# Optimization experiments

Measured on AMD Instinct MI355X. Metric: run time of the kernel, lower is better.

The kernel has to match this reference:

```python
import jax, jax.numpy as jnp
import numpy as np
from jax import lax

DIM = 128
NUM_HEADS = 8
GROUP_SPLIT = (4, 4)
DIM_HEAD = DIM // NUM_HEADS  # 16
SCALOR = DIM_HEAD ** (-0.5)
KSIZE = 5
WS = 4
C_HI = GROUP_SPLIT[0] * DIM_HEAD  # 64
C_LO = GROUP_SPLIT[1] * DIM_HEAD  # 64


def conv1x1(x, w, b):
    # x: [b,c,h,w], w: [o,c], b: [o]
    return jnp.einsum('oc,bchw->bohw', w, x) + b[None, :, None, None]


def dwconv(x, w, b):
    # depthwise conv, w: [C,1,k,k]
    C = x.shape[1]
    pad = KSIZE // 2
    y = lax.conv_general_dilated(x, w, window_strides=(1, 1),
                                 padding=((pad, pad), (pad, pad)),
                                 dimension_numbers=('NCHW', 'OIHW', 'NCHW'),
                                 feature_group_count=C)
    return y + b[None, :, None, None]


def avgpool(x, ws):
    b, c, h, w = x.shape
    return x.reshape(b, c, h // ws, ws, w // ws, ws).mean(axis=(3, 5))


def setup_inputs() -> dict:
    key = jax.random.key(0)
    ks = jax.random.split(key, 16)
    s = 0.02
    inp = {
        'x': jax.random.normal(ks[0], (8, DIM, 96, 96), dtype=jnp.float32),
        'qkv_w': jax.random.normal(ks[1], (3 * C_HI, DIM), dtype=jnp.float32) * s,
        'qkv_b': jnp.zeros((3 * C_HI,), jnp.float32),
        'dw_w': jax.random.normal(ks[2], (3 * C_HI, 1, KSIZE, KSIZE), dtype=jnp.float32) * s,
        'dw_b': jnp.zeros((3 * C_HI,), jnp.float32),
        'am_w1': jax.random.normal(ks[3], (C_HI, C_HI), dtype=jnp.float32) * s,
        'am_b1': jnp.zeros((C_HI,), jnp.float32),
        'am_w2': jax.random.normal(ks[4], (C_HI, C_HI), dtype=jnp.float32) * s,
        'am_b2': jnp.zeros((C_HI,), jnp.float32),
        'gq_w': jax.random.normal(ks[5], (C_LO, DIM), dtype=jnp.float32) * s,
        'gq_b': jnp.zeros((C_LO,), jnp.float32),
        'gkv_w': jax.random.normal(ks[6], (2 * C_LO, DIM), dtype=jnp.float32) * s,
        'gkv_b': jnp.zeros((2 * C_LO,), jnp.float32),
        'proj_w': jax.random.normal(ks[7], (DIM, DIM), dtype=jnp.float32) * s,
        'proj_b': jnp.zeros((DIM,), jnp.float32),
    }
    return inp


def reference(x, qkv_w, qkv_b, dw_w, dw_b, am_w1, am_b1, am_w2, am_b2,
              gq_w, gq_b, gkv_w, gkv_b, proj_w, proj_b):
    b, c, h, w = x.shape
    # ---- high-frequency branch ----
    qkv = dwconv(conv1x1(x, qkv_w, qkv_b), dw_w, dw_b)  # [b, 3*C_HI, h, w]
    qkv = qkv.reshape(b, 3, C_HI, h, w)
    q, k, v = qkv[:, 0], qkv[:, 1], qkv[:, 2]
    a = conv1x1(q * k, am_w1, am_b1)
    a = a * jax.nn.sigmoid(a)  # swish
    a = conv1x1(a, am_w2, am_b2) * SCALOR
    hi = jnp.tanh(a) * v  # [b, C_HI, h, w]
    # ---- low-frequency (windowed global) branch ----
    nq = h * w
    nk = nq // (WS * WS)
    q = conv1x1(x, gq_w, gq_b).reshape(b, GROUP_SPLIT[1], DIM_HEAD, nq)
    q = q.transpose(0, 1, 3, 2)  # [b, H, nq, dh]
    kv = conv1x1(avgpool(x, WS), gkv_w, gkv_b)  # [b, 2*C_LO, h/ws, w/ws]
    kv = kv.reshape(b, 2, GROUP_SPLIT[1], DIM_HEAD, nk)
    kk = kv[:, 0].transpose(0, 1, 3, 2)  # [b, H, nk, dh]
    vv = kv[:, 1].transpose(0, 1, 3, 2)
    attn = jax.nn.softmax(SCALOR * jnp.einsum('bhqd,bhkd->bhqk', q, kk), axis=-1)
    lo = jnp.einsum('bhqk,bhkd->bhqd', attn, vv)  # [b, H, nq, dh]
    lo = lo.transpose(0, 1, 3, 2).reshape(b, C_LO, h, w)
    # ---- merge + projection ----
    out = jnp.concatenate([hi, lo], axis=1)
    return conv1x1(out, proj_w, proj_b)
```

## Files before the change

### kernel.cpp

```cpp
#include <hip/hip_runtime.h>
#include <hip/hip_bf16.h>
#include <hip/hip_fp16.h>
#include <cstdint>

static constexpr int NB  = 8;
static constexpr int HH  = 96;
static constexpr int WW  = 96;
static constexpr int NP  = 9216;
static constexpr int NPK = 576;

using bf8 = __attribute__((ext_vector_type(8))) short;
using f4  = __attribute__((ext_vector_type(4))) float;

__device__ __forceinline__ unsigned pack_bf2(float a, float b) {
    __hip_bfloat162 h = __float22bfloat162_rn(make_float2(a, b));
    unsigned u; __builtin_memcpy(&u, &h, 4);
    return u;
}
__device__ __forceinline__ unsigned short f2bfu(float f) {
    __hip_bfloat16 h = __float2bfloat16(f);
    unsigned short u; __builtin_memcpy(&u, &h, 2);
    return u;
}
__device__ __forceinline__ float bf2f(unsigned short u) {
    unsigned v = (unsigned)u << 16;
    float f; __builtin_memcpy(&f, &v, 4);
    return f;
}
__device__ __forceinline__ float bflo(unsigned p) {
    unsigned v = p << 16; float f; __builtin_memcpy(&f, &v, 4); return f;
}
__device__ __forceinline__ float bfhi(unsigned p) {
    unsigned v = p & 0xffff0000u; float f; __builtin_memcpy(&f, &v, 4); return f;
}

__global__ __launch_bounds__(256) void k_qkvgq(
    const float* __restrict__ x,
    const float* __restrict__ qkv_w, const float* __restrict__ qkv_b,
    const float* __restrict__ gq_w,  const float* __restrict__ gq_b,
    unsigned short* __restrict__ qkv_out,
    unsigned short* __restrict__ gq_out)
{
    __shared__ __align__(16) unsigned xl[64 * 64];
    const int tid  = threadIdx.x;
    const int lane = tid & 63, wid = tid >> 6;
    const int quad = blockIdx.x, b = blockIdx.z;
    const int arow = lane & 15, agrp = lane >> 4;

    const float* xb = x + (long long)b * 128 * NP + quad * 64;

#pragma unroll
    for (int it = 0; it < 4; ++it) {
        const int task = tid + 256 * it;
        const int cp = task >> 4, pq = task & 15;
        float4 a = *(const float4*)&xb[(long long)(2 * cp) * NP + pq * 4];
        float4 c = *(const float4*)&xb[(long long)(2 * cp + 1) * NP + pq * 4];
        const int cps = cp ^ ((pq & 7) << 2);
        xl[(pq * 4 + 0) * 64 + cps] = pack_bf2(a.x, c.x);
        xl[(pq * 4 + 1) * 64 + cps] = pack_bf2(a.y, c.y);
        xl[(pq * 4 + 2) * 64 + cps] = pack_bf2(a.z, c.z);
        xl[(pq * 4 + 3) * 64 + cps] = pack_bf2(a.w, c.w);
    }
    __syncthreads();

    uint4 breg[4][4];
#pragma unroll
    for (int kt = 0; kt < 4; ++kt)
#pragma unroll
        for (int i = 0; i < 4; ++i) {
            const int px = arow * 4 + i;
            const int cp = (kt * 16 + agrp * 4) ^ ((arow & 7) << 2);
            breg[kt][i] = *(const uint4*)&xl[px * 64 + cp];
        }

    for (int gi = 0; gi < 4; ++gi) {
        const int grp = wid + gi * 4;
        const bool isgq = grp >= 12;
        const float* wsrc = isgq ? gq_w : qkv_w;
        const float* bsrc = isgq ? gq_b : qkv_b;
        const float wsc = isgq ? 0.25f : 1.0f;
        const int och = (isgq ? grp - 12 : grp) * 16;

        bf8 afr[4];
#pragma unroll
        for (int kt = 0; kt < 4; ++kt) {
            const float* wp = wsrc + (long long)(och + arow) * 128 + kt * 32 + agrp * 8;
            int4 t;
            t.x = (int)pack_bf2(wp[0] * wsc, wp[1] * wsc);
            t.y = (int)pack_bf2(wp[2] * wsc, wp[3] * wsc);
            t.z = (int)pack_bf2(wp[4] * wsc, wp[5] * wsc);
            t.w = (int)pack_bf2(wp[6] * wsc, wp[7] * wsc);
            afr[kt] = __builtin_bit_cast(bf8, t);
        }

        f4 acc[4];
#pragma unroll
        for (int i = 0; i < 4; ++i) acc[i] = (f4){0.f, 0.f, 0.f, 0.f};
#pragma unroll
        for (int kt = 0; kt < 4; ++kt)
#pragma unroll
            for (int i = 0; i < 4; ++i)
                acc[i] = __builtin_amdgcn_mfma_f32_16x16x32_bf16(
                    afr[kt], __builtin_bit_cast(bf8, breg[kt][i]), acc[i], 0, 0, 0);

        unsigned short* ob = isgq ? gq_out : qkv_out;
        const int ostride = isgq ? 64 : 192;
#pragma unroll
        for (int r = 0; r < 4; ++r) {
            const int o = och + agrp * 4 + r;
            const float bs = bsrc[o] * wsc;
            const float v0 = acc[0][r] + bs, v1 = acc[1][r] + bs;
            const float v2 = acc[2][r] + bs, v3 = acc[3][r] + bs;
            *(uint2*)&ob[((long long)b * ostride + o) * NP + quad * 64 + arow * 4] =
                make_uint2(pack_bf2(v0, v1), pack_bf2(v2, v3));
        }
    }
}

template<int C, int OT, int INBF, int OUTBF>
__global__ __launch_bounds__(256) void k_mfma_conv(
    const void* __restrict__ in0v, const float* __restrict__ w,
    const float* __restrict__ bias, void* __restrict__ outv,
    int np, long long ibs, int storeO, float wscale)
{
    constexpr int KT = C / 32;
    const int tid  = threadIdx.x;
    const int lane = tid & 63, wid = tid >> 6;
    const int b    = blockIdx.z;
    const int obq  = blockIdx.y * (OT * 16);
    const int arow = lane & 15, agrp = lane >> 4;
    const int nquad = np >> 6;

    bf8 afr[OT][KT];
#pragma unroll
    for (int ot = 0; ot < OT; ++ot)
#pragma unroll
        for (int kt = 0; kt < KT; ++kt) {
            const float* wp = w + (long long)(obq + ot * 16 + arow) * C + kt * 32 + agrp * 8;
            int4 t;
            t.x = (int)pack_bf2(wp[0] * wscale, wp[1] * wscale);
            t.y = (int)pack_bf2(wp[2] * wscale, wp[3] * wscale);
            t.z = (int)pack_bf2(wp[4] * wscale, wp[5] * wscale);
            t.w = (int)pack_bf2(wp[6] * wscale, wp[7] * wscale);
            afr[ot][kt] = __builtin_bit_cast(bf8, t);
        }

    const float*          x0f = (const float*)in0v          + (long long)b * (INBF ? 0 : ibs);
    const unsigned short* x0h = (const unsigned short*)in0v + (long long)b * (INBF ? ibs : 0);

    const int quad = blockIdx.x * 4 + wid;
    if (quad >= nquad) return;
    const int p0 = quad * 64 + arow * 4;

    f4 acc[4][OT];
#pragma unroll
    for (int i = 0; i < 4; ++i)
#pragma unroll
        for (int ot = 0; ot < OT; ++ot) acc[i][ot] = (f4){0.f, 0.f, 0.f, 0.f};

#pragma unroll
    for (int kt = 0; kt < KT; ++kt) {
        const long long cbase = kt * 32 + agrp * 8;
        int uu[4][4];
#pragma unroll
        for (int jj = 0; jj < 4; ++jj) {
            if (INBF == 0) {
                float4 a0 = *(const float4*)&x0f[(cbase + 2 * jj) * np + p0];
                float4 a1 = *(const float4*)&x0f[(cbase + 2 * jj + 1) * np + p0];
                uu[0][jj] = (int)pack_bf2(a0.x, a1.x);
                uu[1][jj] = (int)pack_bf2(a0.y, a1.y);
                uu[2][jj] = (int)pack_bf2(a0.z, a1.z);
                uu[3][jj] = (int)pack_bf2(a0.w, a1.w);
            } else {
                ushort4 a0 = *(const ushort4*)&x0h[(cbase + 2 * jj) * np + p0];
                ushort4 a1 = *(const ushort4*)&x0h[(cbase + 2 * jj + 1) * np + p0];
                uu[0][jj] = (int)((unsigned)a0.x | ((unsigned)a1.x << 16));
                uu[1][jj] = (int)((unsigned)a0.y | ((unsigned)a1.y << 16));
                uu[2][jj] = (int)((unsigned)a0.z | ((unsigned)a1.z << 16));
                uu[3][jj] = (int)((unsigned)a0.w | ((unsigned)a1.w << 16));
            }
        }
#pragma unroll
        for (int i = 0; i < 4; ++i) {
            int4 ti = {uu[i][0], uu[i][1], uu[i][2], uu[i][3]};
            bf8 bfr = __builtin_bit_cast(bf8, ti);
#pragma unroll
            for (int ot = 0; ot < OT; ++ot)
                acc[i][ot] = __builtin_amdgcn_mfma_f32_16x16x32_bf16(afr[ot][kt], bfr, acc[i][ot], 0, 0, 0);
        }
    }

#pragma unroll
    for (int ot = 0; ot < OT; ++ot) {
#pragma unroll
        for (int r = 0; r < 4; ++r) {
            const int o = obq + ot * 16 + agrp * 4 + r;
            const float bs = bias[o] * wscale;
            float4 v;
            v.x = acc[0][ot][r] + bs;
            v.y = acc[1][ot][r] + bs;
            v.z = acc[2][ot][r] + bs;
            v.w = acc[3][ot][r] + bs;
            const long long idx = ((long long)b * storeO + o) * np + p0;
            if (OUTBF == 0) {
                *(float4*)&((float*)outv)[idx] = v;
            } else {
                *(uint2*)&((unsigned short*)outv)[idx] =
                    make_uint2(pack_bf2(v.x, v.y), pack_bf2(v.z, v.w));
            }
        }
    }
}

__global__ __launch_bounds__(256) void k_am_fused(
    const unsigned short* __restrict__ dw,
    const float* __restrict__ w1, const float* __restrict__ b1v,
    const float* __restrict__ w2, const float* __restrict__ b2v,
    unsigned short* __restrict__ hi)
{
    __shared__ __align__(16) uint2 abuf[4][1024];

    const int tid  = threadIdx.x;
    const int lane = tid & 63, wid = tid >> 6;
    const int b    = blockIdx.z;
    const int arow = lane & 15, agrp = lane >> 4;

    bf8 afr1[4][2], afr2[4][2];
#pragma unroll
    for (int ot = 0; ot < 4; ++ot)
#pragma unroll
        for (int kt = 0; kt < 2; ++kt) {
            const float* wp1 = w1 + (long long)(ot * 16 + arow) * 64 + kt * 32 + agrp * 8;
            const float* wp2 = w2 + (long long)(ot * 16 + arow) * 64 + kt * 32 + agrp * 8;
            int4 t1, t2;
            t1.x = (int)pack_bf2(wp1[0], wp1[1]);  t2.x = (int)pack_bf2(wp2[0], wp2[1]);
            t1.y = (int)pack_bf2(wp1[2], wp1[3]);  t2.y = (int)pack_bf2(wp2[2], wp2[3]);
            t1.z = (int)pack_bf2(wp1[4], wp1[5]);  t2.z = (int)pack_bf2(wp2[4], wp2[5]);
            t1.w = (int)pack_bf2(wp1[6], wp1[7]);  t2.w = (int)pack_bf2(wp2[6], wp2[7]);
            afr1[ot][kt] = __builtin_bit_cast(bf8, t1);
            afr2[ot][kt] = __builtin_bit_cast(bf8, t2);
        }

    const unsigned short* xq = dw + (long long)b * (192ll * NP);
    const unsigned short* xk = xq + 64ll * NP;
    const unsigned short* xv = xq + 128ll * NP;

    const int quad = blockIdx.x * 4 + wid;
    const int p0 = quad * 64 + arow * 4;

    f4 acc1[4][4];
#pragma unroll
    for (int i = 0; i < 4; ++i)
#pragma unroll
        for (int ot = 0; ot < 4; ++ot) acc1[i][ot] = (f4){0.f, 0.f, 0.f, 0.f};

#pragma unroll
    for (int kt = 0; kt < 2; ++kt) {
        const long long cbase = kt * 32 + agrp * 8;
        int uu[4][4];
#pragma unroll
        for (int jj = 0; jj < 4; ++jj) {
            ushort4 a0 = *(const ushort4*)&xq[(cbase + 2 * jj) * NP + p0];
            ushort4 a1 = *(const ushort4*)&xq[(cbase + 2 * jj + 1) * NP + p0];
            ushort4 y0 = *(const ushort4*)&xk[(cbase + 2 * jj) * NP + p0];
            ushort4 y1 = *(const ushort4*)&xk[(cbase + 2 * jj + 1) * NP + p0];
            uu[0][jj] = (int)pack_bf2(bf2f(a0.x) * bf2f(y0.x), bf2f(a1.x) * bf2f(y1.x));
            uu[1][jj] = (int)pack_bf2(bf2f(a0.y) * bf2f(y0.y), bf2f(a1.y) * bf2f(y1.y));
            uu[2][jj] = (int)pack_bf2(bf2f(a0.z) * bf2f(y0.z), bf2f(a1.z) * bf2f(y1.z));
            uu[3][jj] = (int)pack_bf2(bf2f(a0.w) * bf2f(y0.w), bf2f(a1.w) * bf2f(y1.w));
        }
#pragma unroll
        for (int i = 0; i < 4; ++i) {
            int4 ti = {uu[i][0], uu[i][1], uu[i][2], uu[i][3]};
            bf8 bfr = __builtin_bit_cast(bf8, ti);
#pragma unroll
            for (int ot = 0; ot < 4; ++ot)
                acc1[i][ot] = __builtin_amdgcn_mfma_f32_16x16x32_bf16(afr1[ot][kt], bfr, acc1[i][ot], 0, 0, 0);
        }
    }

#pragma unroll
    for (int i = 0; i < 4; ++i)
#pragma unroll
        for (int ot = 0; ot < 4; ++ot) {
            const int ch0 = ot * 16 + agrp * 4;
            float v0 = acc1[i][ot][0] + b1v[ch0 + 0];
            float v1 = acc1[i][ot][1] + b1v[ch0 + 1];
            float v2 = acc1[i][ot][2] + b1v[ch0 + 2];
            float v3 = acc1[i][ot][3] + b1v[ch0 + 3];
            v0 = v0 / (1.f + __expf(-v0));
            v1 = v1 / (1.f + __expf(-v1));
            v2 = v2 / (1.f + __expf(-v2));
            v3 = v3 / (1.f + __expf(-v3));
            const int c2 = ot * 4 + agrp;
            abuf[wid][(arow * 4 + i) * 16 + (c2 ^ arow)] =
                make_uint2(pack_bf2(v0, v1), pack_bf2(v2, v3));
        }

    f4 acc2[4][4];
#pragma unroll
    for (int i = 0; i < 4; ++i)
#pragma unroll
        for (int ot = 0; ot < 4; ++ot) acc2[i][ot] = (f4){0.f, 0.f, 0.f, 0.f};

#pragma unroll
    for (int kt = 0; kt < 2; ++kt) {
        const int bc2 = kt * 8 + agrp * 2;
#pragma unroll
        for (int i = 0; i < 4; ++i) {
            const uint2 rA = abuf[wid][(arow * 4 + i) * 16 + (bc2 ^ arow)];
            const uint2 rB = abuf[wid][(arow * 4 + i) * 16 + ((bc2 + 1) ^ arow)];
            int4 ti = make_int4((int)rA.x, (int)rA.y, (int)rB.x, (int)rB.y);
            bf8 bfr = __builtin_bit_cast(bf8, ti);
#pragma unroll
            for (int ot = 0; ot < 4; ++ot)
                acc2[i][ot] = __builtin_amdgcn_mfma_f32_16x16x32_bf16(afr2[ot][kt], bfr, acc2[i][ot], 0, 0, 0);
        }
    }

#pragma unroll
    for (int ot = 0; ot < 4; ++ot) {
#pragma unroll
        for (int r = 0; r < 4; ++r) {
            const int o = ot * 16 + agrp * 4 + r;
            const float bs = b2v[o];
            ushort4 vv4 = *(const ushort4*)&xv[(long long)o * NP + p0];
            float h0 = tanhf((acc2[0][ot][r] + bs) * 0.25f) * bf2f(vv4.x);
            float h1 = tanhf((acc2[1][ot][r] + bs) * 0.25f) * bf2f(vv4.y);
            float h2 = tanhf((acc2[2][ot][r] + bs) * 0.25f) * bf2f(vv4.z);
            float h3 = tanhf((acc2[3][ot][r] + bs) * 0.25f) * bf2f(vv4.w);
            *(uint2*)&hi[((long long)b * 128 + o) * NP + p0] =
                make_uint2(pack_bf2(h0, h1), pack_bf2(h2, h3));
        }
    }
}

__global__ __launch_bounds__(256) void k_dwconv5_lds(
    const unsigned short* __restrict__ in, const float* __restrict__ w,
    const float* __restrict__ bias, unsigned short* __restrict__ out, int ch_total)
{
    __shared__ __align__(16) float img[NP];
    const int tid = threadIdx.x;
    const int ch  = blockIdx.x;
    const int b   = blockIdx.y;
    const unsigned short* ip = in + ((long long)b * ch_total + ch) * NP;

#pragma unroll
    for (int j = 0; j < 9; ++j) {
        const uint2 rr = ((const uint2*)ip)[tid + 256 * j];
        float4 f;
        f.x = bflo(rr.x); f.y = bfhi(rr.x);
        f.z = bflo(rr.y); f.w = bfhi(rr.y);
        ((float4*)img)[tid + 256 * j] = f;
    }
    __syncthreads();

    const float* wp = w + ch * 25;
    float wr[25];
#pragma unroll
    for (int i = 0; i < 25; ++i) wr[i] = wp[i];
    const float bs = bias[ch];

    unsigned short* op = out + ((long long)b * ch_total + ch) * NP;

#pragma unroll
    for (int j = 0; j < 9; ++j) {
        const int q  = tid + 256 * j;
        const int y  = q / 24;
        const int x4 = (q - y * 24) * 4;
        float o0 = bs, o1 = bs, o2 = bs, o3 = bs;
#pragma unroll
        for (int ky = 0; ky < 5; ++ky) {
            const int yy = y + ky - 2;
            if (yy < 0 || yy >= HH) continue;
            const float* row = &img[yy * WW + x4];
            float4 mid = *(const float4*)row;
            float4 lf  = (x4 >= 4)      ? *(const float4*)(row - 4)
                                        : make_float4(0.f, 0.f, 0.f, 0.f);
            float4 rt  = (x4 + 4 < WW)  ? *(const float4*)(row + 4)
                                        : make_float4(0.f, 0.f, 0.f, 0.f);
            const float f0 = lf.z,  f1 = lf.w;
            const float f2 = mid.x, f3 = mid.y, f4v = mid.z, f5 = mid.w;
            const float f6 = rt.x,  f7 = rt.y;
            const float w0 = wr[ky * 5 + 0], w1 = wr[ky * 5 + 1],
                        w2 = wr[ky * 5 + 2], w3 = wr[ky * 5 + 3],
                        w4 = wr[ky * 5 + 4];
            o0 = fmaf(w0, f0, o0); o0 = fmaf(w1, f1, o0); o0 = fmaf(w2, f2, o0);
            o0 = fmaf(w3, f3, o0); o0 = fmaf(w4, f4v, o0);
            o1 = fmaf(w0, f1, o1); o1 = fmaf(w1, f2, o1); o1 = fmaf(w2, f3, o1);
            o1 = fmaf(w3, f4v, o1); o1 = fmaf(w4, f5, o1);
            o2 = fmaf(w0, f2, o2); o2 = fmaf(w1, f3, o2); o2 = fmaf(w2, f4v, o2);
            o2 = fmaf(w3, f5, o2); o2 = fmaf(w4, f6, o2);
            o3 = fmaf(w0, f3, o3); o3 = fmaf(w1, f4v, o3); o3 = fmaf(w2, f5, o3);
            o3 = fmaf(w3, f6, o3); o3 = fmaf(w4, f7, o3);
        }
        *(uint2*)&op[y * WW + x4] = make_uint2(pack_bf2(o0, o1), pack_bf2(o2, o3));
    }
}

__global__ __launch_bounds__(256) void k_avgpool4(
    const float* __restrict__ in, float* __restrict__ out)
{
    int idx = blockIdx.x * 256 + threadIdx.x;
    int total = NB * 128 * NPK;
    if (idx >= total) return;
    int pw = idx % 24;
    int t  = idx / 24;
    int ph = t % 24;  t /= 24;
    int c  = t % 128;
    int b  = t / 128;
    const float* ip = in + ((long long)b * 128 + c) * NP + (ph * 4) * WW + pw * 4;
    float s = 0.f;
#pragma unroll
    for (int i = 0; i < 4; ++i)
#pragma unroll
        for (int j = 0; j < 4; ++j) s += ip[i * WW + j];
    out[idx] = s * (1.0f / 16.0f);
}

__global__ __launch_bounds__(256) void k_attn_mfma(
    const unsigned short* __restrict__ q,
    const float* __restrict__ kv,
    unsigned short* __restrict__ hilo)
{
    __shared__ __align__(16) int4  klds4[36 * 32];
    __shared__ __align__(16) int4  zlds4[32];
    __shared__ __align__(16) int4  vlds4[18 * 64];
    __shared__ __align__(16) uint2 elds2[2][4 * 256];

    const int tid  = threadIdx.x;
    const int lane = tid & 63, wid = tid >> 6;
    const int g    = lane >> 4, qi = lane & 15;
    const int bh   = blockIdx.y, b = bh >> 2, h = bh & 3;

    const float* kbase = kv + ((long long)b * 128 + h * 16) * NPK;
    const float* vbase = kv + ((long long)b * 128 + 64 + h * 16) * NPK;

    for (int i = tid; i < 1152; i += 256) {
        const int key = i >> 1, dg = i & 1;
        const float* kp = kbase + (long long)(dg * 8) * NPK + key;
        int4 t;
        t.x = (int)pack_bf2(kp[0],       kp[NPK]);
        t.y = (int)pack_bf2(kp[2 * NPK], kp[3 * NPK]);
        t.z = (int)pack_bf2(kp[4 * NPK], kp[5 * NPK]);
        t.w = (int)pack_bf2(kp[6 * NPK], kp[7 * NPK]);
        klds4[(key >> 4) * 32 + dg * 16 + (key & 15)] = t;
    }
    for (int i = tid; i < 1152; i += 256) {
        const int t = i >> 6, l = i & 63;
        const float* vp = vbase + (long long)(l & 15) * NPK + t * 32 + (l >> 4) * 8;
        float4 a = *(const float4*)vp;
        float4 c = *(const float4*)(vp + 4);
        int4 tt;
        tt.x = (int)pack_bf2(a.x, a.y);
        tt.y = (int)pack_bf2(a.z, a.w);
        tt.z = (int)pack_bf2(c.x, c.y);
        tt.w = (int)pack_bf2(c.z, c.w);
        vlds4[i] = tt;
    }
    if (tid < 32) zlds4[tid] = make_int4(0, 0, 0, 0);
    __syncthreads();

    const int q0 = (blockIdx.x * 4 + wid) * 32;
    const unsigned short* qcol = q + ((long long)b * 64 + h * 16) * NP + q0 + qi;
    int4 qv[2] = { make_int4(0, 0, 0, 0), make_int4(0, 0, 0, 0) };
    if (g < 2) {
#pragma unroll
        for (int s = 0; s < 2; ++s) {
            const unsigned short* qp = qcol + s * 16 + (long long)(g * 8) * NP;
            qv[s].x = (int)((unsigned)qp[0]          | ((unsigned)qp[(long long)NP]     << 16));
            qv[s].y = (int)((unsigned)qp[2ll * NP]   | ((unsigned)qp[3ll * NP]          << 16));
            qv[s].z = (int)((unsigned)qp[4ll * NP]   | ((unsigned)qp[5ll * NP]          << 16));
            qv[s].w = (int)((unsigned)qp[6ll * NP]   | ((unsigned)qp[7ll * NP]          << 16));
        }
    }

    f4 accp[2] = { (f4){0.f, 0.f, 0.f, 0.f}, (f4){0.f, 0.f, 0.f, 0.f} };
    float den[2] = { 0.f, 0.f };

    auto QKEXP = [&](int k2, int buf) {
#pragma unroll
        for (int tp = 0; tp < 2; ++tp) {
            const int4 kf = (lane < 32) ? klds4[(k2 * 2 + tp) * 32 + lane]
                                        : zlds4[lane & 31];
            const bf8 ka = __builtin_bit_cast(bf8, kf);
#pragma unroll
            for (int s = 0; s < 2; ++s) {
                f4 sa = __builtin_amdgcn_mfma_f32_16x16x32_bf16(
                    ka, __builtin_bit_cast(bf8, qv[s]), (f4){0.f, 0.f, 0.f, 0.f}, 0, 0, 0);
                const float e0 = __expf(sa[0]), e1 = __expf(sa[1]);
                const float e2 = __expf(sa[2]), e3 = __expf(sa[3]);
                den[s] += (e0 + e1) + (e2 + e3);
                elds2[buf][wid * 256 + s * 128 + tp * 64 + g * 16 + qi] =
                    make_uint2(pack_bf2(e0, e1), pack_bf2(e2, e3));
            }
        }
    };
    auto PV = [&](int k2, int buf) {
        const bf8 va = __builtin_bit_cast(bf8, vlds4[k2 * 64 + lane]);
#pragma unroll
        for (int s = 0; s < 2; ++s) {
            const int base = wid * 256 + s * 128 + (g >> 1) * 64 + (g & 1) * 32 + qi;
            const uint2 r0 = elds2[buf][base];
            const uint2 r1 = elds2[buf][base + 16];
            int4 ti = make_int4((int)r0.x, (int)r0.y, (int)r1.x, (int)r1.y);
            accp[s] = __builtin_amdgcn_mfma_f32_16x16x32_bf16(
                va, __builtin_bit_cast(bf8, ti), accp[s], 0, 0, 0);
        }
    };

    QKEXP(0, 0);
    for (int k2 = 0; k2 < 17; ++k2) {
        QKEXP(k2 + 1, (k2 + 1) & 1);
        PV(k2, k2 & 1);
    }
    PV(17, 1);

#pragma unroll
    for (int s = 0; s < 2; ++s) {
        float d0 = den[s];
        d0 += __shfl_xor(d0, 16, 64);
        d0 += __shfl_xor(d0, 32, 64);
        const float inv = 1.0f / d0;
        unsigned short* op = hilo + ((long long)b * 128 + 64 + h * 16 + g * 4) * NP + q0 + s * 16 + qi;
#pragma unroll
        for (int r = 0; r < 4; ++r)
            op[(long long)r * NP] = f2bfu(accp[s][r] * inv);
    }
}

extern "C" void kernel_launch(void* const* d_in, const int* in_sizes, int n_in,
                              void* d_out, int out_size, void* d_ws, size_t ws_size,
                              hipStream_t stream)
{
    const float* x      = (const float*)d_in[0];
    const float* qkv_w  = (const float*)d_in[1];
    const float* qkv_b  = (const float*)d_in[2];
    const float* dw_w   = (const float*)d_in[3];
    const float* dw_b   = (const float*)d_in[4];
    const float* am_w1  = (const float*)d_in[5];
    const float* am_b1  = (const float*)d_in[6];
    const float* am_w2  = (const float*)d_in[7];
    const float* am_b2  = (const float*)d_in[8];
    const float* gq_w   = (const float*)d_in[9];
    const float* gq_b   = (const float*)d_in[10];
    const float* gkv_w  = (const float*)d_in[11];
    const float* gkv_b  = (const float*)d_in[12];
    const float* proj_w = (const float*)d_in[13];
    const float* proj_b = (const float*)d_in[14];
    float* out = (float*)d_out;
    char* wsb = (char*)d_ws;

    unsigned short* t_qkv  = (unsigned short*)wsb;
    unsigned short* t_hilo = (unsigned short*)wsb;
    unsigned short* t_dw   = (unsigned short*)(wsb + 28311552);
    unsigned short* t_gq   = (unsigned short*)(wsb + 56623104);
    float*          t_pool = (float*)(wsb + 66060288);
    float*          t_gkv  = (float*)(wsb + 68419584);

    k_qkvgq<<<dim3(144, 1, NB), 256, 0, stream>>>(
        x, qkv_w, qkv_b, gq_w, gq_b, t_qkv, t_gq);
    k_dwconv5_lds<<<dim3(192, NB), 256, 0, stream>>>(t_qkv, dw_w, dw_b, t_dw, 192);
    k_avgpool4<<<dim3((NB*128*NPK + 255)/256), 256, 0, stream>>>(x, t_pool);
    k_mfma_conv<128,4,0,0><<<dim3(3,2,NB), 256, 0, stream>>>(
        t_pool, gkv_w, gkv_b, t_gkv, NPK, (long long)128 * NPK, 128, 1.0f);
    k_am_fused<<<dim3(36,1,NB), 256, 0, stream>>>(
        t_dw, am_w1, am_b1, am_w2, am_b2, t_hilo);
    k_attn_mfma<<<dim3(72, 32), 256, 0, stream>>>(t_gq, t_gkv, t_hilo);
    k_mfma_conv<128,4,1,0><<<dim3(36,2,NB), 256, 0, stream>>>(
        t_hilo, proj_w, proj_b, out, NP, (long long)128 * NP, 128, 1.0f);
}
```

Before: 172.2 us.

## Double queries per wave in attention kernel and drop software pipelining

Each wave now handles 64 queries instead of 32, so the K/V tiles staged in LDS per block are reused across twice as many queries and the grid is halved. The double-buffered QK/PV software pipeline is replaced by a single-buffer loop whose LDS exp buffer is written and then read by the same wave. The zero-fill LDS array is replaced by a register select. This amortizes K/V staging and conversion but doubles register pressure and removes the overlap between exp computation and the PV MFMAs.

```diff
diff --git a/kernel.cpp b/kernel.cpp
--- a/kernel.cpp
+++ b/kernel.cpp
@@ -424,9 +424,8 @@
     unsigned short* __restrict__ hilo)
 {
     __shared__ __align__(16) int4  klds4[36 * 32];
-    __shared__ __align__(16) int4  zlds4[32];
     __shared__ __align__(16) int4  vlds4[18 * 64];
-    __shared__ __align__(16) uint2 elds2[2][4 * 256];
+    __shared__ __align__(16) uint2 elds2[4 * 512];
 
     const int tid  = threadIdx.x;
     const int lane = tid & 63, wid = tid >> 6;
@@ -458,66 +457,59 @@
         tt.w = (int)pack_bf2(c.z, c.w);
         vlds4[i] = tt;
     }
-    if (tid < 32) zlds4[tid] = make_int4(0, 0, 0, 0);
     __syncthreads();
 
-    const int q0 = (blockIdx.x * 4 + wid) * 32;
+    const int q0 = (blockIdx.x * 4 + wid) * 64;
     const unsigned short* qcol = q + ((long long)b * 64 + h * 16) * NP + q0 + qi;
-    int4 qv[2] = { make_int4(0, 0, 0, 0), make_int4(0, 0, 0, 0) };
+    int4 qv[4] = { make_int4(0,0,0,0), make_int4(0,0,0,0),
+                   make_int4(0,0,0,0), make_int4(0,0,0,0) };
     if (g < 2) {
 #pragma unroll
-        for (int s = 0; s < 2; ++s) {
+        for (int s = 0; s < 4; ++s) {
             const unsigned short* qp = qcol + s * 16 + (long long)(g * 8) * NP;
-            qv[s].x = (int)((unsigned)qp[0]          | ((unsigned)qp[(long long)NP]     << 16));
-            qv[s].y = (int)((unsigned)qp[2ll * NP]   | ((unsigned)qp[3ll * NP]          << 16));
-            qv[s].z = (int)((unsigned)qp[4ll * NP]   | ((unsigned)qp[5ll * NP]          << 16));
-            qv[s].w = (int)((unsigned)qp[6ll * NP]   | ((unsigned)qp[7ll * NP]          << 16));
-        }
-    }
-
-    f4 accp[2] = { (f4){0.f, 0.f, 0.f, 0.f}, (f4){0.f, 0.f, 0.f, 0.f} };
-    float den[2] = { 0.f, 0.f };
-
-    auto QKEXP = [&](int k2, int buf) {
+            qv[s].x = (int)((unsigned)qp[0]        | ((unsigned)qp[(long long)NP] << 16));
+            qv[s].y = (int)((unsigned)qp[2ll * NP] | ((unsigned)qp[3ll * NP]      << 16));
+            qv[s].z = (int)((unsigned)qp[4ll * NP] | ((unsigned)qp[5ll * NP]      << 16));
+            qv[s].w = (int)((unsigned)qp[6ll * NP] | ((unsigned)qp[7ll * NP]      << 16));
+        }
+    }
+
+    f4 accp[4] = { (f4){0.f,0.f,0.f,0.f}, (f4){0.f,0.f,0.f,0.f},
+                   (f4){0.f,0.f,0.f,0.f}, (f4){0.f,0.f,0.f,0.f} };
+    float den[4] = { 0.f, 0.f, 0.f, 0.f };
+    const int wb = wid * 512;
+
+    for (int k2 = 0; k2 < 18; ++k2) {
 #pragma unroll
         for (int tp = 0; tp < 2; ++tp) {
-            const int4 kf = (lane < 32) ? klds4[(k2 * 2 + tp) * 32 + lane]
-                                        : zlds4[lane & 31];
+            int4 kf = klds4[(k2 * 2 + tp) * 32 + (lane & 31)];
+            if (lane >= 32) kf = make_int4(0, 0, 0, 0);
             const bf8 ka = __builtin_bit_cast(bf8, kf);
 #pragma unroll
-            for (int s = 0; s < 2; ++s) {
+            for (int s = 0; s < 4; ++s) {
                 f4 sa = __builtin_amdgcn_mfma_f32_16x16x32_bf16(
                     ka, __builtin_bit_cast(bf8, qv[s]), (f4){0.f, 0.f, 0.f, 0.f}, 0, 0, 0);
                 const float e0 = __expf(sa[0]), e1 = __expf(sa[1]);
                 const float e2 = __expf(sa[2]), e3 = __expf(sa[3]);
                 den[s] += (e0 + e1) + (e2 + e3);
-                elds2[buf][wid * 256 + s * 128 + tp * 64 + g * 16 + qi] =
+                elds2[wb + s * 128 + tp * 64 + g * 16 + qi] =
                     make_uint2(pack_bf2(e0, e1), pack_bf2(e2, e3));
             }
         }
-    };
-    auto PV = [&](int k2, int buf) {
         const bf8 va = __builtin_bit_cast(bf8, vlds4[k2 * 64 + lane]);
 #pragma unroll
-        for (int s = 0; s < 2; ++s) {
-            const int base = wid * 256 + s * 128 + (g >> 1) * 64 + (g & 1) * 32 + qi;
-            const uint2 r0 = elds2[buf][base];
-            const uint2 r1 = elds2[buf][base + 16];
+        for (int s = 0; s < 4; ++s) {
+            const int base = wb + s * 128 + (g >> 1) * 64 + (g & 1) * 32 + qi;
+            const uint2 r0 = elds2[base];
+            const uint2 r1 = elds2[base + 16];
             int4 ti = make_int4((int)r0.x, (int)r0.y, (int)r1.x, (int)r1.y);
             accp[s] = __builtin_amdgcn_mfma_f32_16x16x32_bf16(
                 va, __builtin_bit_cast(bf8, ti), accp[s], 0, 0, 0);
         }
-    };
-
-    QKEXP(0, 0);
-    for (int k2 = 0; k2 < 17; ++k2) {
-        QKEXP(k2 + 1, (k2 + 1) & 1);
-        PV(k2, k2 & 1);
-    }
-    PV(17, 1);
-
-#pragma unroll
-    for (int s = 0; s < 2; ++s) {
+    }
+
+#pragma unroll
+    for (int s = 0; s < 4; ++s) {
         float d0 = den[s];
         d0 += __shfl_xor(d0, 16, 64);
         d0 += __shfl_xor(d0, 32, 64);
@@ -566,7 +558,7 @@
         t_pool, gkv_w, gkv_b, t_gkv, NPK, (long long)128 * NPK, 128, 1.0f);
     k_am_fused<<<dim3(36,1,NB), 256, 0, stream>>>(
         t_dw, am_w1, am_b1, am_w2, am_b2, t_hilo);
-    k_attn_mfma<<<dim3(72, 32), 256, 0, stream>>>(t_gq, t_gkv, t_hilo);
+    k_attn_mfma<<<dim3(36, 32), 256, 0, stream>>>(t_gq, t_gkv, t_hilo);
     k_mfma_conv<128,4,1,0><<<dim3(36,2,NB), 256, 0, stream>>>(
         t_hilo, proj_w, proj_b, out, NP, (long long)128 * NP, 128, 1.0f);
 }
```

After: 173.9 us. No clear change (+1.0%).

## Fold log2e into query weights, compute softmax denominator via MFMA, vectorize avgpool

Applied to the files above, without the earlier changes.

Scales the gq weights by scale*log2(e) so the attention kernel can use exp2 directly, dropping the per-element multiply inside expf. The softmax denominator is no longer a scalar sum plus cross-lane shuffles; it comes from an extra MFMA against a vector of ones, which also makes it consistent with the bf16-rounded probabilities. The loop also gets s_setprio hints, and avgpool reads rows as float4. The cost is extra MFMA work per PV step and slightly different numerics.

```diff
diff --git a/kernel.cpp b/kernel.cpp
--- a/kernel.cpp
+++ b/kernel.cpp
@@ -78,7 +78,7 @@
         const bool isgq = grp >= 12;
         const float* wsrc = isgq ? gq_w : qkv_w;
         const float* bsrc = isgq ? gq_b : qkv_b;
-        const float wsc = isgq ? 0.25f : 1.0f;
+        const float wsc = isgq ? 0.36067376022224085f : 1.0f;
         const int och = (isgq ? grp - 12 : grp) * 16;
 
         bf8 afr[4];
@@ -410,11 +410,12 @@
     int c  = t % 128;
     int b  = t / 128;
     const float* ip = in + ((long long)b * 128 + c) * NP + (ph * 4) * WW + pw * 4;
-    float s = 0.f;
-#pragma unroll
-    for (int i = 0; i < 4; ++i)
-#pragma unroll
-        for (int j = 0; j < 4; ++j) s += ip[i * WW + j];
+    float4 r0 = *(const float4*)(ip);
+    float4 r1 = *(const float4*)(ip + WW);
+    float4 r2 = *(const float4*)(ip + 2 * WW);
+    float4 r3 = *(const float4*)(ip + 3 * WW);
+    float s = ((r0.x + r0.y) + (r0.z + r0.w)) + ((r1.x + r1.y) + (r1.z + r1.w))
+            + ((r2.x + r2.y) + (r2.z + r2.w)) + ((r3.x + r3.y) + (r3.z + r3.w));
     out[idx] = s * (1.0f / 16.0f);
 }
 
@@ -475,8 +476,11 @@
         }
     }
 
+    const bf8 ones = { (short)0x3F80, (short)0x3F80, (short)0x3F80, (short)0x3F80,
+                       (short)0x3F80, (short)0x3F80, (short)0x3F80, (short)0x3F80 };
+
     f4 accp[2] = { (f4){0.f, 0.f, 0.f, 0.f}, (f4){0.f, 0.f, 0.f, 0.f} };
-    float den[2] = { 0.f, 0.f };
+    f4 dacc[2] = { (f4){0.f, 0.f, 0.f, 0.f}, (f4){0.f, 0.f, 0.f, 0.f} };
 
     auto QKEXP = [&](int k2, int buf) {
 #pragma unroll
@@ -488,11 +492,9 @@
             for (int s = 0; s < 2; ++s) {
                 f4 sa = __builtin_amdgcn_mfma_f32_16x16x32_bf16(
                     ka, __builtin_bit_cast(bf8, qv[s]), (f4){0.f, 0.f, 0.f, 0.f}, 0, 0, 0);
-                const float e0 = __expf(sa[0]), e1 = __expf(sa[1]);
-                const float e2 = __expf(sa[2]), e3 = __expf(sa[3]);
-                den[s] += (e0 + e1) + (e2 + e3);
                 elds2[buf][wid * 256 + s * 128 + tp * 64 + g * 16 + qi] =
-                    make_uint2(pack_bf2(e0, e1), pack_bf2(e2, e3));
+                    make_uint2(pack_bf2(exp2f(sa[0]), exp2f(sa[1])),
+                               pack_bf2(exp2f(sa[2]), exp2f(sa[3])));
             }
         }
     };
@@ -506,22 +508,23 @@
             int4 ti = make_int4((int)r0.x, (int)r0.y, (int)r1.x, (int)r1.y);
             accp[s] = __builtin_amdgcn_mfma_f32_16x16x32_bf16(
                 va, __builtin_bit_cast(bf8, ti), accp[s], 0, 0, 0);
+            dacc[s] = __builtin_amdgcn_mfma_f32_16x16x32_bf16(
+                ones, __builtin_bit_cast(bf8, ti), dacc[s], 0, 0, 0);
         }
     };
 
     QKEXP(0, 0);
     for (int k2 = 0; k2 < 17; ++k2) {
+        __builtin_amdgcn_s_setprio(1);
         QKEXP(k2 + 1, (k2 + 1) & 1);
         PV(k2, k2 & 1);
+        __builtin_amdgcn_s_setprio(0);
     }
     PV(17, 1);
 
 #pragma unroll
     for (int s = 0; s < 2; ++s) {
-        float d0 = den[s];
-        d0 += __shfl_xor(d0, 16, 64);
-        d0 += __shfl_xor(d0, 32, 64);
-        const float inv = 1.0f / d0;
+        const float inv = 1.0f / dacc[s][0];
         unsigned short* op = hilo + ((long long)b * 128 + 64 + h * 16 + g * 4) * NP + q0 + s * 16 + qi;
 #pragma unroll
         for (int r = 0; r < 4; ++r)
```

After: 187.2 us. 8.7% more time.
